# Performance work log

Hardware: AMD Instinct MI355X
Metric: run time of the kernel (lower is better)

Reference implementation:

```python
import jax, jax.numpy as jnp
import numpy as np

B, T, E, D = 4, 1024, 1024, 2048   # batch, dec len, enc len, model dim
N, K, H = 16, 8, 256               # q heads, kv heads, head dim
G = N // K                         # GQA group size
SCALE = H ** -0.5                  # query_pre_attn_scalar
SOFT_CAP = 50.0
EPS = 1e-6
ROPE_BASE = 10000.0
_K_MASK = jnp.finfo(jnp.bfloat16).min


def _rms_norm(x, scale, eps=EPS):
    var = jnp.mean(jnp.square(x), axis=-1, keepdims=True)
    return x * jax.lax.rsqrt(var + eps) * (1.0 + scale)


def _apply_rope(x, positions, base=ROPE_BASE):
    # x: [B, L, n, H], positions: [B, L]; rope_proportion=1.0, scale_factor=1.0
    h = x.shape[-1]
    freq_exp = 2.0 / h * jnp.arange(h // 2, dtype=jnp.float32)
    timescale = base ** freq_exp                                  # [H/2]
    ang = (positions.astype(jnp.float32)[..., None] / timescale)[..., None, :]  # [B,L,1,H/2]
    sin, cos = jnp.sin(ang), jnp.cos(ang)
    x1, x2 = jnp.split(x, 2, axis=-1)
    out = jnp.concatenate([x1 * cos - x2 * sin, x2 * cos + x1 * sin], axis=-1)
    return out.astype(x.dtype)


def setup_inputs() -> dict:
    key = jax.random.key(0)
    ks = jax.random.split(key, 8)
    hidden_states = jax.random.normal(ks[0], (B, T, D), jnp.float32)
    encoder_hidden_states = jax.random.normal(ks[1], (B, E, D), jnp.float32)
    position_ids = jnp.broadcast_to(jnp.arange(T, dtype=jnp.int32)[None, :], (B, T))
    # merged mask: causal over self part, full visibility over cross part
    causal = jnp.tril(jnp.ones((T, T), jnp.bool_))
    cross = jnp.ones((T, E), jnp.bool_)
    merged_attention_mask = jnp.broadcast_to(
        jnp.concatenate([causal, cross], axis=-1)[None, None], (B, 1, T, T + E))
    w = 0.02
    q_w = jax.random.normal(ks[2], (N, D, H), jnp.float32) * w
    k_w = jax.random.normal(ks[3], (K, D, H), jnp.float32) * w
    v_w = jax.random.normal(ks[4], (K, D, H), jnp.float32) * w
    o_w = jax.random.normal(ks[5], (N, H, D), jnp.float32) * w
    q_scale = jax.random.normal(ks[6], (H,), jnp.float32) * w
    k_scale = jax.random.normal(ks[7], (H,), jnp.float32) * w
    return dict(hidden_states=hidden_states, encoder_hidden_states=encoder_hidden_states,
                position_ids=position_ids, merged_attention_mask=merged_attention_mask,
                q_w=q_w, k_w=k_w, v_w=v_w, o_w=o_w, q_scale=q_scale, k_scale=k_scale)


def reference(hidden_states, encoder_hidden_states, position_ids, merged_attention_mask,
              q_w, k_w, v_w, o_w, q_scale, k_scale):
    # QKV projections
    query = jnp.einsum('BTD,NDH->BTNH', hidden_states, q_w)
    self_key = jnp.einsum('BTD,KDH->BTKH', hidden_states, k_w)
    self_value = jnp.einsum('BTD,KDH->BTKH', hidden_states, v_w)
    # QK-RMSNorm
    query = _rms_norm(query, q_scale)
    self_key = _rms_norm(self_key, k_scale)
    # RoPE on self-attention q/k only
    query = _apply_rope(query, position_ids)
    self_key = _apply_rope(self_key, position_ids)
    # Cross K/V from encoder states (no RoPE)
    cross_key = _rms_norm(jnp.einsum('BTD,KDH->BTKH', encoder_hidden_states, k_w), k_scale)
    cross_value = jnp.einsum('BTD,KDH->BTKH', encoder_hidden_states, v_w)
    # Merge self + cross along key axis
    keys = jnp.concatenate([self_key, cross_key], axis=1)       # [B, T+E, K, H]
    values = jnp.concatenate([self_value, cross_value], axis=1)
    # Scaled GQA attention
    q = (query * SCALE).reshape(B, T, K, G, H)
    logits = jnp.einsum('BTKGH,BSKH->BKGTS', q, keys)
    # logit soft-capping
    logits = SOFT_CAP * jnp.tanh(logits / SOFT_CAP)
    mask = merged_attention_mask[:, :, None]                    # [B,1,1,T,S]
    logits = jnp.where(mask, logits, _K_MASK)
    probs = jax.nn.softmax(logits.astype(jnp.float32), axis=-1).astype(keys.dtype)
    attn = jnp.einsum('BKGTS,BSKH->BTKGH', probs, values).reshape(B, T, N, H)
    return jnp.einsum('BTNH,NHD->BTD', attn, o_w)
```

## Files before the change

kernel.cpp:

```cpp
#include <hip/hip_runtime.h>
#include <hip/hip_bf16.h>
#include <cstdio>


typedef __attribute__((ext_vector_type(8))) short bf16x8;
typedef __attribute__((ext_vector_type(4))) float f32x4;

static __device__ __forceinline__ ushort f2bf(float x){
  uint u = __float_as_uint(x);
  u += 0x7fffu + ((u >> 16) & 1u);
  return (ushort)(u >> 16);
}
static __device__ __forceinline__ float bf2f(ushort u){
  return __uint_as_float((uint)u << 16);
}
#define GLL16(gp, lp)                                                          \
  __builtin_amdgcn_global_load_lds(                                            \
      (const __attribute__((address_space(1))) void*)(gp),                     \
      (__attribute__((address_space(3))) void*)(lp), 16, 0, 0)

__global__ void k_detect(const uint* __restrict__ src, int* __restrict__ flag){
  int lane = threadIdx.x & 63;
  int cnt = 0;
  for (int i = 0; i < 4; i++){
    uint w = src[lane * 4 + i];
    uint e = (w >> 7) & 0xffu;
    cnt += (e >= 90u && e <= 141u) ? 1 : 0;
  }
  for (int o = 1; o < 64; o <<= 1) cnt += __shfl_xor(cnt, o);
  if (lane == 0) *flag = (cnt >= 128) ? 1 : 0;
}

__global__ void k_tobf(const void* __restrict__ src, ushort* __restrict__ dst,
                       int n8, const int* __restrict__ flag){
  int i = blockIdx.x * blockDim.x + threadIdx.x;
  if (i >= n8) return;
  if (*flag){
    reinterpret_cast<uint4*>(dst)[i] = reinterpret_cast<const uint4*>(src)[i];
  } else {
    const float4* s = reinterpret_cast<const float4*>(src);
    float4 a = s[i * 2], b = s[i * 2 + 1];
    ushort o[8] = { f2bf(a.x), f2bf(a.y), f2bf(a.z), f2bf(a.w),
                    f2bf(b.x), f2bf(b.y), f2bf(b.z), f2bf(b.w) };
    reinterpret_cast<uint4*>(dst)[i] = *reinterpret_cast<uint4*>(o);
  }
}

__global__ void k_wtrans(const void* __restrict__ in, ushort* __restrict__ out,
                         int R, int C, const int* __restrict__ flag){
  __shared__ ushort t[32][33];
  int isbf = *flag;
  int p = blockIdx.z;
  int r0 = blockIdx.y * 32, c0 = blockIdx.x * 32;
  ushort* op = out + (size_t)p * R * C;
  int cc = threadIdx.x & 31, rr = threadIdx.x >> 5;
  if (isbf){
    const ushort* ip = (const ushort*)in + (size_t)p * R * C;
    for (int i = 0; i < 32; i += 8)
      t[rr + i][cc] = ip[(size_t)(r0 + rr + i) * C + c0 + cc];
  } else {
    const float* ip = (const float*)in + (size_t)p * R * C;
    for (int i = 0; i < 32; i += 8)
      t[rr + i][cc] = f2bf(ip[(size_t)(r0 + rr + i) * C + c0 + cc]);
  }
  __syncthreads();
  for (int i = 0; i < 32; i += 8)
    op[(size_t)(c0 + rr + i) * R + r0 + cc] = t[cc][rr + i];
}

template<int EPI, typename OutT>
__global__ __launch_bounds__(256)
void k_gemm_bt(const ushort* __restrict__ A0, const ushort* __restrict__ A1, int Msplit,
               const ushort* __restrict__ Bm, OutT* __restrict__ Cout,
               int M, int N, int Kd){
  __shared__ ushort As[128 * 32];
  __shared__ ushort Bs[128 * 32];
  const int tid = threadIdx.x;
  const int m0 = blockIdx.y * 128, n0 = blockIdx.x * 128;
  const ushort* Ap = (m0 < Msplit) ? (A0 + (size_t)m0 * Kd)
                                   : (A1 + (size_t)(m0 - Msplit) * Kd);
  const ushort* Bp = Bm + (size_t)n0 * Kd;
  const int w = tid >> 6, lane = tid & 63, c = lane & 15, q = lane >> 4;
  const int wr = (w >> 1) * 64, wc = (w & 1) * 64;

  f32x4 zf = {0.f, 0.f, 0.f, 0.f};
  f32x4 acc[4][4];
  for (int mi = 0; mi < 4; mi++) for (int ni = 0; ni < 4; ni++) acc[mi][ni] = zf;

  const int sr = tid >> 2, sc8 = (tid & 3) * 8;
  const ushort* ga = Ap + (size_t)sr * Kd + sc8;
  const ushort* gb = Bp + (size_t)sr * Kd + sc8;
  ushort* la = &As[sr * 32 + sc8];
  ushort* lb = &Bs[sr * 32 + sc8];
  const size_t rowskip = (size_t)64 * Kd;

  for (int k0 = 0; k0 < Kd; k0 += 32){
    GLL16(ga + k0,           la);
    GLL16(ga + k0 + rowskip, la + 64 * 32);
    GLL16(gb + k0,           lb);
    GLL16(gb + k0 + rowskip, lb + 64 * 32);
    __syncthreads();
    bf16x8 af[4], bfrg[4];
    for (int mi = 0; mi < 4; mi++)
      af[mi] = *reinterpret_cast<const bf16x8*>(&As[(wr + mi * 16 + c) * 32 + q * 8]);
    for (int ni = 0; ni < 4; ni++)
      bfrg[ni] = *reinterpret_cast<const bf16x8*>(&Bs[(wc + ni * 16 + c) * 32 + q * 8]);
    for (int mi = 0; mi < 4; mi++)
      for (int ni = 0; ni < 4; ni++)
        acc[mi][ni] = __builtin_amdgcn_mfma_f32_16x16x32_bf16(af[mi], bfrg[ni], acc[mi][ni], 0, 0, 0);
    __syncthreads();
  }

  for (int mi = 0; mi < 4; mi++)
    for (int ni = 0; ni < 4; ni++){
      int gr0 = m0 + wr + mi * 16 + q * 4;
      int gc  = n0 + wc + ni * 16 + c;
      if constexpr (EPI == 0){
        for (int r = 0; r < 4; r++){
          if constexpr (sizeof(OutT) == 2)
            Cout[(size_t)(gr0 + r) * N + gc] = (OutT)f2bf(acc[mi][ni][r]);
          else
            Cout[(size_t)(gr0 + r) * N + gc] = (OutT)acc[mi][ni][r];
        }
      } else if constexpr (EPI == 1){
        for (int r = 0; r < 4; r++){
          int gr = gr0 + r, b, s;
          if (gr < 4096){ b = gr >> 10; s = gr & 1023; }
          else { int g2 = gr - 4096; b = g2 >> 10; s = 1024 + (g2 & 1023); }
          Cout[(size_t)(b * 2048 + s) * N + gc] = (OutT)f2bf(acc[mi][ni][r]);
        }
      } else {
        int gr = gr0, b, s;
        if (gr < 4096){ b = gr >> 10; s = gr & 1023; }
        else { int g2 = gr - 4096; b = g2 >> 10; s = 1024 + (g2 & 1023); }
        int kk = gc >> 8, h = gc & 255;
        ushort4 o;
        o.x = f2bf(acc[mi][ni][0]); o.y = f2bf(acc[mi][ni][1]);
        o.z = f2bf(acc[mi][ni][2]); o.w = f2bf(acc[mi][ni][3]);
        *reinterpret_cast<ushort4*>((ushort*)Cout + ((size_t)(b * 8 + kk) * 256 + h) * 2048 + s) = o;
      }
    }
}

__global__ __launch_bounds__(256)
void k_norm_q(const ushort* __restrict__ Qraw, const int* __restrict__ pos,
              const ushort* __restrict__ scale, ushort* __restrict__ Qbf){
  int w = threadIdx.x >> 6, lane = threadIdx.x & 63;
  int gw = blockIdx.x * 4 + w;
  int bt = gw >> 4;
  ushort4 xu = *reinterpret_cast<const ushort4*>(Qraw + (size_t)gw * 256 + lane * 4);
  float x[4] = { bf2f(xu.x), bf2f(xu.y), bf2f(xu.z), bf2f(xu.w) };
  float ss = x[0]*x[0] + x[1]*x[1] + x[2]*x[2] + x[3]*x[3];
  for (int o = 32; o > 0; o >>= 1) ss += __shfl_xor(ss, o);
  float rin = rsqrtf(ss * (1.f / 256.f) + 1e-6f);
  ushort4 su = *reinterpret_cast<const ushort4*>(scale + lane * 4);
  float y[4] = { x[0] * rin * (1.f + bf2f(su.x)), x[1] * rin * (1.f + bf2f(su.y)),
                 x[2] * rin * (1.f + bf2f(su.z)), x[3] * rin * (1.f + bf2f(su.w)) };
  float oth[4];
  for (int i = 0; i < 4; i++) oth[i] = __shfl_xor(y[i], 32);
  bool hi = lane >= 32;
  float fb = (float)((lane & 31) * 4);
  float p = (float)pos[bt];
  ushort4 o;
  ushort* op[4] = {&o.x, &o.y, &o.z, &o.w};
  for (int i = 0; i < 4; i++){
    float fi = fb + i;
    float tsi = expf(fi * -0.07195578415f);
    float ang = p * tsi;
    float sn, cs; sincosf(ang, &sn, &cs);
    float v = hi ? (y[i] * cs + oth[i] * sn) : (y[i] * cs - oth[i] * sn);
    *op[i] = f2bf(v * 0.0625f);
  }
  *reinterpret_cast<ushort4*>(Qbf + (size_t)gw * 256 + lane * 4) = o;
}

__global__ __launch_bounds__(256)
void k_norm_k(const ushort* __restrict__ Kraw, const int* __restrict__ pos,
              const ushort* __restrict__ scale, ushort* __restrict__ Kbf){
  int w = threadIdx.x >> 6, lane = threadIdx.x & 63;
  int gw = blockIdx.x * 4 + w;
  int row = gw >> 3;
  int s = row & 2047, b = row >> 11;
  ushort4 xu = *reinterpret_cast<const ushort4*>(Kraw + (size_t)gw * 256 + lane * 4);
  float x[4] = { bf2f(xu.x), bf2f(xu.y), bf2f(xu.z), bf2f(xu.w) };
  float ss = x[0]*x[0] + x[1]*x[1] + x[2]*x[2] + x[3]*x[3];
  for (int o = 32; o > 0; o >>= 1) ss += __shfl_xor(ss, o);
  float rin = rsqrtf(ss * (1.f / 256.f) + 1e-6f);
  ushort4 su = *reinterpret_cast<const ushort4*>(scale + lane * 4);
  float y[4] = { x[0] * rin * (1.f + bf2f(su.x)), x[1] * rin * (1.f + bf2f(su.y)),
                 x[2] * rin * (1.f + bf2f(su.z)), x[3] * rin * (1.f + bf2f(su.w)) };
  ushort4 o;
  ushort* op[4] = {&o.x, &o.y, &o.z, &o.w};
  if (s < 1024){
    float oth[4];
    for (int i = 0; i < 4; i++) oth[i] = __shfl_xor(y[i], 32);
    bool hi = lane >= 32;
    float fb = (float)((lane & 31) * 4);
    float p = (float)pos[b * 1024 + s];
    for (int i = 0; i < 4; i++){
      float fi = fb + i;
      float tsi = expf(fi * -0.07195578415f);
      float ang = p * tsi;
      float sn, cs; sincosf(ang, &sn, &cs);
      float v = hi ? (y[i] * cs + oth[i] * sn) : (y[i] * cs - oth[i] * sn);
      *op[i] = f2bf(v);
    }
  } else {
    for (int i = 0; i < 4; i++) *op[i] = f2bf(y[i]);
  }
  *reinterpret_cast<ushort4*>(Kbf + (size_t)gw * 256 + lane * 4) = o;
}

__global__ __launch_bounds__(256)
void k_attn(const ushort* __restrict__ Qbf, const ushort* __restrict__ Kbf,
            const ushort* __restrict__ Vt, ushort* __restrict__ attn){
  constexpr int KSs = 264, VSs = 40, PSs = 40;
  __shared__ ushort Ks[32 * KSs];
  __shared__ ushort Vs[256 * VSs];
  __shared__ ushort Pm[4][16 * PSs];
  int id = blockIdx.x;
  int xcd = id & 7, slot = id >> 3;
  int grp = xcd + 8 * (slot >> 5);
  int within = slot & 31;
  int b = grp >> 3, kk = grp & 7;
  int n = kk * 2 + (within >> 4);
  int t0 = (within & 15) * 64;
  int tid = threadIdx.x, w = tid >> 6, lane = tid & 63, c = lane & 15, q = lane >> 4;

  bf16x8 qf[8];
  {
    int tq = t0 + w * 16 + c;
    const ushort* qp = Qbf + ((size_t)(b * 1024 + tq) * 16 + n) * 256 + q * 8;
    for (int f = 0; f < 8; f++) qf[f] = *reinterpret_cast<const bf16x8*>(qp + f * 32);
  }
  f32x4 zf = {0.f, 0.f, 0.f, 0.f};
  f32x4 accO[16];
  for (int i = 0; i < 16; i++) accO[i] = zf;
  float lacc[4] = {0.f, 0.f, 0.f, 0.f};

  const ushort* Kbase = Kbf + ((size_t)b * 2048 * 8 + kk) * 256;
  const ushort* Vbase = Vt + (size_t)(b * 8 + kk) * 256 * 2048;
  int nself = (t0 >> 5) + 2;
  int ntile = nself + 32;
  for (int it = 0; it < ntile; ++it){
    int s0 = (it < nself) ? it * 32 : 1024 + (it - nself) * 32;
    for (int i = 0; i < 4; i++){
      int tau = tid + i * 256;
      int r = tau >> 5, ch = (tau & 31) * 8;
      *reinterpret_cast<uint4*>(&Ks[r * KSs + ch]) =
        *reinterpret_cast<const uint4*>(Kbase + (size_t)(s0 + r) * 2048 + ch);
    }
    for (int i = 0; i < 4; i++){
      int tau = tid + i * 256;
      int h = tau >> 2, ch = (tau & 3) * 8;
      *reinterpret_cast<uint4*>(&Vs[h * VSs + ch]) =
        *reinterpret_cast<const uint4*>(Vbase + (size_t)h * 2048 + s0 + ch);
    }
    __syncthreads();
    f32x4 accL[2]; accL[0] = zf; accL[1] = zf;
    for (int ni = 0; ni < 2; ni++)
      for (int f = 0; f < 8; f++){
        bf16x8 kb = *reinterpret_cast<const bf16x8*>(&Ks[(ni * 16 + c) * KSs + f * 32 + q * 8]);
        accL[ni] = __builtin_amdgcn_mfma_f32_16x16x32_bf16(qf[f], kb, accL[ni], 0, 0, 0);
      }
    ushort* pw = Pm[w];
    for (int ni = 0; ni < 2; ni++)
      for (int r = 0; r < 4; r++){
        int s = s0 + ni * 16 + c;
        int t = t0 + w * 16 + q * 4 + r;
        float x = accL[ni][r] * 0.02f;
        float xc = fminf(fmaxf(x, -10.f), 10.f);
        float e2 = __expf(2.f * xc);
        float l2 = 50.f * (1.f - 2.f / (e2 + 1.f));
        float pv = (s >= 1024 || s <= t) ? __expf(l2) : 0.f;
        lacc[r] += pv;
        pw[(q * 4 + r) * PSs + ni * 16 + c] = f2bf(pv);
      }
    __asm__ volatile("s_waitcnt lgkmcnt(0)" ::: "memory");
    bf16x8 pa = *reinterpret_cast<const bf16x8*>(&pw[c * PSs + q * 8]);
    for (int hi = 0; hi < 16; hi++){
      bf16x8 vb = *reinterpret_cast<const bf16x8*>(&Vs[(hi * 16 + c) * VSs + q * 8]);
      accO[hi] = __builtin_amdgcn_mfma_f32_16x16x32_bf16(pa, vb, accO[hi], 0, 0, 0);
    }
    __syncthreads();
  }
  for (int r = 0; r < 4; r++)
    for (int o = 1; o < 16; o <<= 1) lacc[r] += __shfl_xor(lacc[r], o);
  float inv[4];
  for (int r = 0; r < 4; r++) inv[r] = 1.f / fmaxf(lacc[r], 1e-37f);
  for (int hi = 0; hi < 16; hi++)
    for (int r = 0; r < 4; r++){
      int t = t0 + w * 16 + q * 4 + r;
      attn[((size_t)(b * 1024 + t) * 16 + n) * 256 + hi * 16 + c] = f2bf(accO[hi][r] * inv[r]);
    }
}

extern "C" void kernel_launch(void* const* d_in, const int* in_sizes, int n_in,
                              void* d_out, int out_size, void* d_ws, size_t ws_size,
                              hipStream_t stream){
  const void* hidden = d_in[0];
  const void* enc    = d_in[1];
  const int*  posids = (const int*)d_in[2];
  const void* qw = d_in[4];
  const void* kw = d_in[5];
  const void* vw = d_in[6];
  const void* ow = d_in[7];
  const void* qs = d_in[8];
  const void* ks = d_in[9];
  float* out = (float*)d_out;

  char* ws = (char*)d_ws;
  size_t off = 0;
  auto alloc = [&](size_t sz){ void* p = ws + off; off += sz; return p; };
  ushort* Hb  = (ushort*)alloc(16777216);
  ushort* Eb  = (ushort*)alloc(16777216);
  ushort* Wq = (ushort*)alloc(16777216);
  ushort* Wk = (ushort*)alloc(8388608);
  ushort* Wv = (ushort*)alloc(8388608);
  ushort* Wo = (ushort*)alloc(16777216);
  ushort* Qbf = (ushort*)alloc(33554432);
  ushort* Kbf = (ushort*)alloc(33554432);
  char* S1 = (char*)alloc(67108864);
  ushort* qsb = (ushort*)alloc(512);
  ushort* ksb = (ushort*)alloc(512);
  int* flag  = (int*)alloc(64);
  ushort* Qraw = (ushort*)S1;
  ushort* Kraw = (ushort*)S1;
  ushort* Vt   = (ushort*)S1;
  ushort* attnb = (ushort*)(S1 + 33554432);
  if (off > ws_size){
    fprintf(stderr, "kernel_launch: ws too small: need %zu, have %zu\n", off, ws_size);
    return;
  }

  k_detect<<<1, 64, 0, stream>>>((const uint*)hidden, flag);
  k_tobf<<<4096, 256, 0, stream>>>(hidden, Hb, 1048576, flag);
  k_tobf<<<4096, 256, 0, stream>>>(enc,    Eb, 1048576, flag);
  k_tobf<<<1, 256, 0, stream>>>(qs, qsb, 32, flag);
  k_tobf<<<1, 256, 0, stream>>>(ks, ksb, 32, flag);

  k_wtrans<<<dim3(8, 64, 16), 256, 0, stream>>>(qw, Wq, 2048, 256, flag);
  k_wtrans<<<dim3(8, 64, 8),  256, 0, stream>>>(kw, Wk, 2048, 256, flag);
  k_wtrans<<<dim3(8, 64, 8),  256, 0, stream>>>(vw, Wv, 2048, 256, flag);
  k_wtrans<<<dim3(64, 128, 1), 256, 0, stream>>>(ow, Wo, 4096, 2048, flag);

  k_gemm_bt<0, ushort><<<dim3(32, 32), 256, 0, stream>>>(Hb, Hb, 1 << 30, Wq, Qraw, 4096, 4096, 2048);
  k_norm_q<<<16384, 256, 0, stream>>>(Qraw, posids, qsb, Qbf);
  k_gemm_bt<1, ushort><<<dim3(16, 64), 256, 0, stream>>>(Hb, Eb, 4096, Wk, Kraw, 8192, 2048, 2048);
  k_norm_k<<<16384, 256, 0, stream>>>(Kraw, posids, ksb, Kbf);
  k_gemm_bt<2, ushort><<<dim3(16, 64), 256, 0, stream>>>(Hb, Eb, 4096, Wv, Vt, 8192, 2048, 2048);

  k_attn<<<1024, 256, 0, stream>>>(Qbf, Kbf, Vt, attnb);

  k_gemm_bt<0, float><<<dim3(16, 32), 256, 0, stream>>>(attnb, attnb, 1 << 30, Wo, out, 4096, 2048, 4096);
}
```

Measured before the change: 960.0 us.

## Fuse QKV projections into one GEMM and double query rows per attention wave

The Q, K and V projection GEMMs are merged into a single launch over a concatenated weight matrix. Blocks that would compute Q columns for encoder rows exit early, and each column range uses its own epilogue. The attention kernel now has each wave process 32 query rows in two 16-row groups, so every K/V tile loaded into shared memory serves twice as many queries. That halves the block count to 512 and raises register pressure from the doubled accumulators, and the workspace layout is reorganised to alias buffers.

```diff
diff --git a/kernel.cpp b/kernel.cpp
--- a/kernel.cpp
+++ b/kernel.cpp
@@ -68,17 +68,19 @@
     op[(size_t)(c0 + rr + i) * R + r0 + cc] = t[cc][rr + i];
 }
 
-template<int EPI, typename OutT>
 __global__ __launch_bounds__(256)
-void k_gemm_bt(const ushort* __restrict__ A0, const ushort* __restrict__ A1, int Msplit,
-               const ushort* __restrict__ Bm, OutT* __restrict__ Cout,
-               int M, int N, int Kd){
+void k_gemm_qkv(const ushort* __restrict__ A0, const ushort* __restrict__ A1,
+                const ushort* __restrict__ Bm,
+                ushort* __restrict__ Qo, ushort* __restrict__ Ko,
+                ushort* __restrict__ Vo){
+  const int m0 = blockIdx.y * 128, n0 = blockIdx.x * 128;
+  if (n0 < 4096 && m0 >= 4096) return;
   __shared__ ushort As[128 * 32];
   __shared__ ushort Bs[128 * 32];
   const int tid = threadIdx.x;
-  const int m0 = blockIdx.y * 128, n0 = blockIdx.x * 128;
-  const ushort* Ap = (m0 < Msplit) ? (A0 + (size_t)m0 * Kd)
-                                   : (A1 + (size_t)(m0 - Msplit) * Kd);
+  const int Kd = 2048;
+  const ushort* Ap = (m0 < 4096) ? (A0 + (size_t)m0 * Kd)
+                                 : (A1 + (size_t)(m0 - 4096) * Kd);
   const ushort* Bp = Bm + (size_t)n0 * Kd;
   const int w = tid >> 6, lane = tid & 63, c = lane & 15, q = lane >> 4;
   const int wr = (w >> 1) * 64, wc = (w & 1) * 64;
@@ -115,30 +117,73 @@
     for (int ni = 0; ni < 4; ni++){
       int gr0 = m0 + wr + mi * 16 + q * 4;
       int gc  = n0 + wc + ni * 16 + c;
-      if constexpr (EPI == 0){
-        for (int r = 0; r < 4; r++){
-          if constexpr (sizeof(OutT) == 2)
-            Cout[(size_t)(gr0 + r) * N + gc] = (OutT)f2bf(acc[mi][ni][r]);
-          else
-            Cout[(size_t)(gr0 + r) * N + gc] = (OutT)acc[mi][ni][r];
-        }
-      } else if constexpr (EPI == 1){
+      if (n0 < 4096){
+        for (int r = 0; r < 4; r++)
+          Qo[(size_t)(gr0 + r) * 4096 + gc] = f2bf(acc[mi][ni][r]);
+      } else if (n0 < 6144){
+        int col = gc - 4096;
         for (int r = 0; r < 4; r++){
           int gr = gr0 + r, b, s;
           if (gr < 4096){ b = gr >> 10; s = gr & 1023; }
           else { int g2 = gr - 4096; b = g2 >> 10; s = 1024 + (g2 & 1023); }
-          Cout[(size_t)(b * 2048 + s) * N + gc] = (OutT)f2bf(acc[mi][ni][r]);
+          Ko[(size_t)(b * 2048 + s) * 2048 + col] = f2bf(acc[mi][ni][r]);
         }
       } else {
+        int col = gc - 6144;
         int gr = gr0, b, s;
         if (gr < 4096){ b = gr >> 10; s = gr & 1023; }
         else { int g2 = gr - 4096; b = g2 >> 10; s = 1024 + (g2 & 1023); }
-        int kk = gc >> 8, h = gc & 255;
+        int kk = col >> 8, h = col & 255;
         ushort4 o;
         o.x = f2bf(acc[mi][ni][0]); o.y = f2bf(acc[mi][ni][1]);
         o.z = f2bf(acc[mi][ni][2]); o.w = f2bf(acc[mi][ni][3]);
-        *reinterpret_cast<ushort4*>((ushort*)Cout + ((size_t)(b * 8 + kk) * 256 + h) * 2048 + s) = o;
+        *reinterpret_cast<ushort4*>(Vo + ((size_t)(b * 8 + kk) * 256 + h) * 2048 + s) = o;
       }
+    }
+}
+
+__global__ __launch_bounds__(256)
+void k_gemm_o(const ushort* __restrict__ A0, const ushort* __restrict__ Bm,
+              float* __restrict__ Cout, int N, int Kd){
+  __shared__ ushort As[128 * 32];
+  __shared__ ushort Bs[128 * 32];
+  const int tid = threadIdx.x;
+  const int m0 = blockIdx.y * 128, n0 = blockIdx.x * 128;
+  const ushort* Ap = A0 + (size_t)m0 * Kd;
+  const ushort* Bp = Bm + (size_t)n0 * Kd;
+  const int w = tid >> 6, lane = tid & 63, c = lane & 15, q = lane >> 4;
+  const int wr = (w >> 1) * 64, wc = (w & 1) * 64;
+  f32x4 zf = {0.f, 0.f, 0.f, 0.f};
+  f32x4 acc[4][4];
+  for (int mi = 0; mi < 4; mi++) for (int ni = 0; ni < 4; ni++) acc[mi][ni] = zf;
+  const int sr = tid >> 2, sc8 = (tid & 3) * 8;
+  const ushort* ga = Ap + (size_t)sr * Kd + sc8;
+  const ushort* gb = Bp + (size_t)sr * Kd + sc8;
+  ushort* la = &As[sr * 32 + sc8];
+  ushort* lb = &Bs[sr * 32 + sc8];
+  const size_t rowskip = (size_t)64 * Kd;
+  for (int k0 = 0; k0 < Kd; k0 += 32){
+    GLL16(ga + k0,           la);
+    GLL16(ga + k0 + rowskip, la + 64 * 32);
+    GLL16(gb + k0,           lb);
+    GLL16(gb + k0 + rowskip, lb + 64 * 32);
+    __syncthreads();
+    bf16x8 af[4], bfrg[4];
+    for (int mi = 0; mi < 4; mi++)
+      af[mi] = *reinterpret_cast<const bf16x8*>(&As[(wr + mi * 16 + c) * 32 + q * 8]);
+    for (int ni = 0; ni < 4; ni++)
+      bfrg[ni] = *reinterpret_cast<const bf16x8*>(&Bs[(wc + ni * 16 + c) * 32 + q * 8]);
+    for (int mi = 0; mi < 4; mi++)
+      for (int ni = 0; ni < 4; ni++)
+        acc[mi][ni] = __builtin_amdgcn_mfma_f32_16x16x32_bf16(af[mi], bfrg[ni], acc[mi][ni], 0, 0, 0);
+    __syncthreads();
+  }
+  for (int mi = 0; mi < 4; mi++)
+    for (int ni = 0; ni < 4; ni++){
+      int gr0 = m0 + wr + mi * 16 + q * 4;
+      int gc  = n0 + wc + ni * 16 + c;
+      for (int r = 0; r < 4; r++)
+        Cout[(size_t)(gr0 + r) * N + gc] = acc[mi][ni][r];
     }
 }
 
@@ -217,30 +262,31 @@
   constexpr int KSs = 264, VSs = 40, PSs = 40;
   __shared__ ushort Ks[32 * KSs];
   __shared__ ushort Vs[256 * VSs];
-  __shared__ ushort Pm[4][16 * PSs];
+  __shared__ ushort Pm[4][32 * PSs];
   int id = blockIdx.x;
   int xcd = id & 7, slot = id >> 3;
-  int grp = xcd + 8 * (slot >> 5);
-  int within = slot & 31;
+  int grp = xcd + 8 * (slot >> 4);
+  int within = slot & 15;
   int b = grp >> 3, kk = grp & 7;
-  int n = kk * 2 + (within >> 4);
-  int t0 = (within & 15) * 64;
+  int n = kk * 2 + (within >> 3);
+  int t0 = (within & 7) * 128;
   int tid = threadIdx.x, w = tid >> 6, lane = tid & 63, c = lane & 15, q = lane >> 4;
-
-  bf16x8 qf[8];
-  {
-    int tq = t0 + w * 16 + c;
+  int rowbase = t0 + w * 32;
+
+  bf16x8 qf[2][8];
+  for (int g = 0; g < 2; g++){
+    int tq = rowbase + g * 16 + c;
     const ushort* qp = Qbf + ((size_t)(b * 1024 + tq) * 16 + n) * 256 + q * 8;
-    for (int f = 0; f < 8; f++) qf[f] = *reinterpret_cast<const bf16x8*>(qp + f * 32);
+    for (int f = 0; f < 8; f++) qf[g][f] = *reinterpret_cast<const bf16x8*>(qp + f * 32);
   }
   f32x4 zf = {0.f, 0.f, 0.f, 0.f};
-  f32x4 accO[16];
-  for (int i = 0; i < 16; i++) accO[i] = zf;
-  float lacc[4] = {0.f, 0.f, 0.f, 0.f};
+  f32x4 accO[2][16];
+  for (int g = 0; g < 2; g++) for (int i = 0; i < 16; i++) accO[g][i] = zf;
+  float lacc[2][4] = {{0.f,0.f,0.f,0.f},{0.f,0.f,0.f,0.f}};
 
   const ushort* Kbase = Kbf + ((size_t)b * 2048 * 8 + kk) * 256;
   const ushort* Vbase = Vt + (size_t)(b * 8 + kk) * 256 * 2048;
-  int nself = (t0 >> 5) + 2;
+  int nself = (t0 >> 5) + 4;
   int ntile = nself + 32;
   for (int it = 0; it < ntile; ++it){
     int s0 = (it < nself) ? it * 32 : 1024 + (it - nself) * 32;
@@ -257,42 +303,50 @@
         *reinterpret_cast<const uint4*>(Vbase + (size_t)h * 2048 + s0 + ch);
     }
     __syncthreads();
-    f32x4 accL[2]; accL[0] = zf; accL[1] = zf;
+    f32x4 accL[2][2];
+    accL[0][0] = zf; accL[0][1] = zf; accL[1][0] = zf; accL[1][1] = zf;
     for (int ni = 0; ni < 2; ni++)
       for (int f = 0; f < 8; f++){
         bf16x8 kb = *reinterpret_cast<const bf16x8*>(&Ks[(ni * 16 + c) * KSs + f * 32 + q * 8]);
-        accL[ni] = __builtin_amdgcn_mfma_f32_16x16x32_bf16(qf[f], kb, accL[ni], 0, 0, 0);
+        accL[0][ni] = __builtin_amdgcn_mfma_f32_16x16x32_bf16(qf[0][f], kb, accL[0][ni], 0, 0, 0);
+        accL[1][ni] = __builtin_amdgcn_mfma_f32_16x16x32_bf16(qf[1][f], kb, accL[1][ni], 0, 0, 0);
       }
     ushort* pw = Pm[w];
-    for (int ni = 0; ni < 2; ni++)
-      for (int r = 0; r < 4; r++){
-        int s = s0 + ni * 16 + c;
-        int t = t0 + w * 16 + q * 4 + r;
-        float x = accL[ni][r] * 0.02f;
-        float xc = fminf(fmaxf(x, -10.f), 10.f);
-        float e2 = __expf(2.f * xc);
-        float l2 = 50.f * (1.f - 2.f / (e2 + 1.f));
-        float pv = (s >= 1024 || s <= t) ? __expf(l2) : 0.f;
-        lacc[r] += pv;
-        pw[(q * 4 + r) * PSs + ni * 16 + c] = f2bf(pv);
-      }
+    for (int g = 0; g < 2; g++)
+      for (int ni = 0; ni < 2; ni++)
+        for (int r = 0; r < 4; r++){
+          int s = s0 + ni * 16 + c;
+          int t = rowbase + g * 16 + q * 4 + r;
+          float x = accL[g][ni][r] * 0.02f;
+          float xc = fminf(fmaxf(x, -10.f), 10.f);
+          float e2 = __expf(2.f * xc);
+          float l2 = 50.f * (1.f - 2.f / (e2 + 1.f));
+          float pv = (s >= 1024 || s <= t) ? __expf(l2) : 0.f;
+          lacc[g][r] += pv;
+          pw[(g * 16 + q * 4 + r) * PSs + ni * 16 + c] = f2bf(pv);
+        }
     __asm__ volatile("s_waitcnt lgkmcnt(0)" ::: "memory");
-    bf16x8 pa = *reinterpret_cast<const bf16x8*>(&pw[c * PSs + q * 8]);
+    bf16x8 pa0 = *reinterpret_cast<const bf16x8*>(&pw[c * PSs + q * 8]);
+    bf16x8 pa1 = *reinterpret_cast<const bf16x8*>(&pw[(16 + c) * PSs + q * 8]);
     for (int hi = 0; hi < 16; hi++){
       bf16x8 vb = *reinterpret_cast<const bf16x8*>(&Vs[(hi * 16 + c) * VSs + q * 8]);
-      accO[hi] = __builtin_amdgcn_mfma_f32_16x16x32_bf16(pa, vb, accO[hi], 0, 0, 0);
-    }
-    __syncthreads();
-  }
-  for (int r = 0; r < 4; r++)
-    for (int o = 1; o < 16; o <<= 1) lacc[r] += __shfl_xor(lacc[r], o);
-  float inv[4];
-  for (int r = 0; r < 4; r++) inv[r] = 1.f / fmaxf(lacc[r], 1e-37f);
-  for (int hi = 0; hi < 16; hi++)
-    for (int r = 0; r < 4; r++){
-      int t = t0 + w * 16 + q * 4 + r;
-      attn[((size_t)(b * 1024 + t) * 16 + n) * 256 + hi * 16 + c] = f2bf(accO[hi][r] * inv[r]);
-    }
+      accO[0][hi] = __builtin_amdgcn_mfma_f32_16x16x32_bf16(pa0, vb, accO[0][hi], 0, 0, 0);
+      accO[1][hi] = __builtin_amdgcn_mfma_f32_16x16x32_bf16(pa1, vb, accO[1][hi], 0, 0, 0);
+    }
+    __syncthreads();
+  }
+  for (int g = 0; g < 2; g++)
+    for (int r = 0; r < 4; r++)
+      for (int o = 1; o < 16; o <<= 1) lacc[g][r] += __shfl_xor(lacc[g][r], o);
+  for (int g = 0; g < 2; g++){
+    float inv[4];
+    for (int r = 0; r < 4; r++) inv[r] = 1.f / fmaxf(lacc[g][r], 1e-37f);
+    for (int hi = 0; hi < 16; hi++)
+      for (int r = 0; r < 4; r++){
+        int t = rowbase + g * 16 + q * 4 + r;
+        attn[((size_t)(b * 1024 + t) * 16 + n) * 256 + hi * 16 + c] = f2bf(accO[g][hi][r] * inv[r]);
+      }
+  }
 }
 
 extern "C" void kernel_launch(void* const* d_in, const int* in_sizes, int n_in,
@@ -312,22 +366,20 @@
   char* ws = (char*)d_ws;
   size_t off = 0;
   auto alloc = [&](size_t sz){ void* p = ws + off; off += sz; return p; };
-  ushort* Hb  = (ushort*)alloc(16777216);
-  ushort* Eb  = (ushort*)alloc(16777216);
-  ushort* Wq = (ushort*)alloc(16777216);
-  ushort* Wk = (ushort*)alloc(8388608);
-  ushort* Wv = (ushort*)alloc(8388608);
-  ushort* Wo = (ushort*)alloc(16777216);
-  ushort* Qbf = (ushort*)alloc(33554432);
-  ushort* Kbf = (ushort*)alloc(33554432);
-  char* S1 = (char*)alloc(67108864);
-  ushort* qsb = (ushort*)alloc(512);
-  ushort* ksb = (ushort*)alloc(512);
-  int* flag  = (int*)alloc(64);
-  ushort* Qraw = (ushort*)S1;
-  ushort* Kraw = (ushort*)S1;
-  ushort* Vt   = (ushort*)S1;
-  ushort* attnb = (ushort*)(S1 + 33554432);
+  char*   HbEb = (char*)alloc(33554432);
+  ushort* Hb   = (ushort*)HbEb;
+  ushort* Eb   = (ushort*)(HbEb + 16777216);
+  ushort* Wcat = (ushort*)alloc(33554432);
+  ushort* Wo   = (ushort*)alloc(16777216);
+  ushort* Qraw = (ushort*)alloc(33554432);
+  ushort* Kraw = (ushort*)alloc(33554432);
+  ushort* Vt   = (ushort*)alloc(33554432);
+  ushort* qsb  = (ushort*)alloc(512);
+  ushort* ksb  = (ushort*)alloc(512);
+  int*    flag = (int*)alloc(64);
+  ushort* Qbf   = (ushort*)HbEb;
+  ushort* Kbf   = Qraw;
+  ushort* attnb = Kraw;
   if (off > ws_size){
     fprintf(stderr, "kernel_launch: ws too small: need %zu, have %zu\n", off, ws_size);
     return;
@@ -339,18 +391,17 @@
   k_tobf<<<1, 256, 0, stream>>>(qs, qsb, 32, flag);
   k_tobf<<<1, 256, 0, stream>>>(ks, ksb, 32, flag);
 
-  k_wtrans<<<dim3(8, 64, 16), 256, 0, stream>>>(qw, Wq, 2048, 256, flag);
-  k_wtrans<<<dim3(8, 64, 8),  256, 0, stream>>>(kw, Wk, 2048, 256, flag);
-  k_wtrans<<<dim3(8, 64, 8),  256, 0, stream>>>(vw, Wv, 2048, 256, flag);
+  k_wtrans<<<dim3(8, 64, 16), 256, 0, stream>>>(qw, Wcat,            2048, 256, flag);
+  k_wtrans<<<dim3(8, 64, 8),  256, 0, stream>>>(kw, Wcat + 8388608,  2048, 256, flag);
+  k_wtrans<<<dim3(8, 64, 8),  256, 0, stream>>>(vw, Wcat + 12582912, 2048, 256, flag);
   k_wtrans<<<dim3(64, 128, 1), 256, 0, stream>>>(ow, Wo, 4096, 2048, flag);
 
-  k_gemm_bt<0, ushort><<<dim3(32, 32), 256, 0, stream>>>(Hb, Hb, 1 << 30, Wq, Qraw, 4096, 4096, 2048);
+  k_gemm_qkv<<<dim3(64, 64), 256, 0, stream>>>(Hb, Eb, Wcat, Qraw, Kraw, Vt);
+
   k_norm_q<<<16384, 256, 0, stream>>>(Qraw, posids, qsb, Qbf);
-  k_gemm_bt<1, ushort><<<dim3(16, 64), 256, 0, stream>>>(Hb, Eb, 4096, Wk, Kraw, 8192, 2048, 2048);
   k_norm_k<<<16384, 256, 0, stream>>>(Kraw, posids, ksb, Kbf);
-  k_gemm_bt<2, ushort><<<dim3(16, 64), 256, 0, stream>>>(Hb, Eb, 4096, Wv, Vt, 8192, 2048, 2048);
-
-  k_attn<<<1024, 256, 0, stream>>>(Qbf, Kbf, Vt, attnb);
-
-  k_gemm_bt<0, float><<<dim3(16, 32), 256, 0, stream>>>(attnb, attnb, 1 << 30, Wo, out, 4096, 2048, 4096);
-}
+
+  k_attn<<<512, 256, 0, stream>>>(Qbf, Kbf, Vt, attnb);
+
+  k_gemm_o<<<dim3(16, 32), 256, 0, stream>>>(attnb, Wo, out, 2048, 4096);
+}
```

After: 906.1 us. 5.6% less time.
